# Optimization experiments

Hardware: AMD Instinct MI355X
Metric: run time of the kernel (lower is better)

Reference implementation:

```python
import jax, jax.numpy as jnp
import numpy as np

NUM_HEADS = 16

def setup_inputs() -> dict:
    key = jax.random.key(0)
    ks = jax.random.split(key, 8)
    B, S, X, D = 2, 2048, 1, 1024
    scale = 1.0 / np.sqrt(D)
    return {
        "query": jax.random.normal(ks[0], (B, S, X, D), jnp.float32),
        "key": jax.random.normal(ks[1], (B, S, X, D), jnp.float32),
        "value": jax.random.normal(ks[2], (B, S, X, D), jnp.float32),
        "Wq": jax.random.normal(ks[3], (D, D), jnp.float32) * scale,
        "bq": jnp.zeros((D,), jnp.float32),
        "Wk": jax.random.normal(ks[4], (D, D), jnp.float32) * scale,
        "bk": jnp.zeros((D,), jnp.float32),
        "Wv": jax.random.normal(ks[5], (D, D), jnp.float32) * scale,
        "bv": jnp.zeros((D,), jnp.float32),
        "Wo": jax.random.normal(ks[6], (D, D), jnp.float32) * scale,
        "bo": jnp.zeros((D,), jnp.float32),
    }

def _split_heads(x, B, H):
    # [B, S, X, D] -> [B, H, S*X, depth]
    D = x.shape[-1]
    return x.reshape(B, -1, H, D // H).transpose(0, 2, 1, 3)

def reference(query, key, value, Wq, bq, Wk, bk, Wv, bv, Wo, bo):
    B, S, X, D = query.shape
    H = NUM_HEADS
    q = _split_heads(query @ Wq + bq, B, H)   # [B,H,L,dh], L=S*X
    k = _split_heads(key @ Wk + bk, B, H)
    v = _split_heads(value @ Wv + bv, B, H)
    dh = k.shape[-1]
    logits = jnp.einsum("bhqd,bhkd->bhqk", q, k) / jnp.sqrt(jnp.float32(dh))
    attn = jax.nn.softmax(logits, axis=-1)
    out = jnp.einsum("bhqk,bhkd->bhqd", attn, v)   # [B,H,L,dh]
    out = out.transpose(0, 2, 1, 3).reshape(B, S, -1, D)  # [B,S,X,D]
    return out @ Wo + bo
```

## Files before the change

kernel.cpp:

```cpp
#include <hip/hip_runtime.h>
#include <cstdint>
#include <cstddef>

typedef __bf16 bf16x8 __attribute__((ext_vector_type(8)));
typedef float f32x4 __attribute__((ext_vector_type(4)));
typedef float f32x16 __attribute__((ext_vector_type(16)));
typedef unsigned short u16;
typedef unsigned int u32;

static constexpr int Bn = 2;
static constexpr int L  = 2048;
static constexpr int Dm = 1024;
static constexpr int H  = 16;
static constexpr int DH = 64;
static constexpr int M  = Bn * L;
static constexpr size_t PER = (size_t)Bn * H * L * DH;
static constexpr int NQ = Bn * H * L;

#define SC 0.18033688f

__device__ __forceinline__ u16 f2bf(float f) {
    union { float f; u32 u; } v; v.f = f;
    u32 u = v.u + 0x7FFFu + ((v.u >> 16) & 1u);
    return (u16)(u >> 16);
}

__device__ __forceinline__ u32 pk_bf16(float a, float b) {
#if __has_builtin(__builtin_amdgcn_cvt_pk_bf16_f32)
    typedef __bf16 bf16x2_t __attribute__((ext_vector_type(2)));
    bf16x2_t t = __builtin_amdgcn_cvt_pk_bf16_f32(a, b);
    u32 r; __builtin_memcpy(&r, &t, 4); return r;
#else
    return (u32)f2bf(a) | ((u32)f2bf(b) << 16);
#endif
}
__device__ __forceinline__ u16 f2bf1(float f) { return (u16)(pk_bf16(f, f) & 0xffffu); }

__device__ __forceinline__ void gl2lds16(const void* g, void* l) {
    __builtin_amdgcn_global_load_lds(
        (const __attribute__((address_space(1))) u32*)(uintptr_t)g,
        (__attribute__((address_space(3))) u32*)(uintptr_t)l, 16, 0, 0);
}

__global__ __launch_bounds__(256) void convert_in(
    const float* __restrict__ q, const float* __restrict__ k, const float* __restrict__ v,
    u16* __restrict__ dst)
{
    const float* src = (blockIdx.y == 0) ? q : (blockIdx.y == 1) ? k : v;
    u16* d = dst + (size_t)blockIdx.y * M * Dm;
    const size_t t = (size_t)blockIdx.x * 256 + threadIdx.x;
    const float4* s4 = reinterpret_cast<const float4*>(src) + t * 2;
    float4 f0 = s4[0], f1 = s4[1];
    u32 o[4] = { pk_bf16(f0.x, f0.y), pk_bf16(f0.z, f0.w),
                 pk_bf16(f1.x, f1.y), pk_bf16(f1.z, f1.w) };
    reinterpret_cast<uint4*>(d)[t] = *reinterpret_cast<uint4*>(o);
}

__global__ __launch_bounds__(256) void convert_wt(
    const float* __restrict__ Wq, const float* __restrict__ Wk,
    const float* __restrict__ Wv, const float* __restrict__ Wo,
    u16* __restrict__ dst)
{
    __shared__ u16 Ts[64][72];
    const int z = blockIdx.z;
    const float* W = (z == 0) ? Wq : (z == 1) ? Wk : (z == 2) ? Wv : Wo;
    u16* o = dst + (size_t)z * Dm * Dm;
    const int n0 = blockIdx.x * 64, k0 = blockIdx.y * 64;
    const int tid = threadIdx.x;

    {
        const int kr = tid >> 2, nc = (tid & 3) * 16;
        const float* s = W + (size_t)(k0 + kr) * Dm + n0 + nc;
        const float4* s4 = reinterpret_cast<const float4*>(s);
        float4 a = s4[0], b = s4[1], c = s4[2], d = s4[3];
        u32 t[8] = { pk_bf16(a.x, a.y), pk_bf16(a.z, a.w), pk_bf16(b.x, b.y), pk_bf16(b.z, b.w),
                     pk_bf16(c.x, c.y), pk_bf16(c.z, c.w), pk_bf16(d.x, d.y), pk_bf16(d.z, d.w) };
        *reinterpret_cast<uint4*>(&Ts[kr][nc])     = reinterpret_cast<uint4*>(t)[0];
        *reinterpret_cast<uint4*>(&Ts[kr][nc + 8]) = reinterpret_cast<uint4*>(t)[1];
    }
    __syncthreads();
    {
        const int nr = tid >> 2, kc = (tid & 3) * 16;
        u16 w[16];
        #pragma unroll
        for (int j = 0; j < 16; ++j) w[j] = Ts[kc + j][nr];
        u16* dptr = o + (size_t)(n0 + nr) * Dm + k0 + kc;
        *reinterpret_cast<uint4*>(dptr)     = reinterpret_cast<uint4*>(w)[0];
        *reinterpret_cast<uint4*>(dptr + 8) = reinterpret_cast<uint4*>(w)[1];
    }
}

__global__ __launch_bounds__(256) void gemm_qkv(
    const u16* __restrict__ Abuf, const u16* __restrict__ Wtb,
    const float* __restrict__ bq, const float* __restrict__ bk, const float* __restrict__ bv,
    u16* __restrict__ Qh, u16* __restrict__ Kh, u16* __restrict__ Vth)
{
    __shared__ __align__(16) char smem[36864];

    const int tid = threadIdx.x;
    const int wave = tid >> 6, lane = tid & 63;
    const int quad = lane >> 4, l16 = lane & 15;
    const int wr = wave >> 1, wc = wave & 1;
    const int z = blockIdx.z;
    const u16* A  = Abuf + (size_t)z * M * Dm;
    const u16* Bt = Wtb  + (size_t)z * Dm * Dm;
    const float* bias = (z == 0) ? bq : (z == 1) ? bk : bv;
    u16* out = (z == 0) ? Qh : (z == 1) ? Kh : Vth;
    const int n0 = blockIdx.x * 128, m0 = blockIdx.y * 128;

    const int srow = lane >> 2;
    const int skc  = (lane & 3) * 8;

    f32x4 acc[4][4] = {};

    auto stage = [&](int k0, int bi) {
        #pragma unroll
        for (int i = 0; i < 2; ++i) {
            const int ra = i * 64 + wave * 16;
            gl2lds16(A  + (size_t)(m0 + ra + srow) * Dm + k0 + skc, smem + bi * 8192 + ra * 64);
            gl2lds16(Bt + (size_t)(n0 + ra + srow) * Dm + k0 + skc, smem + 16384 + bi * 8192 + ra * 64);
        }
    };

    stage(0, 0);
    for (int k0 = 0, it = 0; k0 < Dm; k0 += 32, ++it) {
        const int cb = it & 1;
        __syncthreads();
        if (k0 + 32 < Dm) stage(k0 + 32, cb ^ 1);
        const u16* Asb = (const u16*)(smem + cb * 8192);
        const u16* Bsb = (const u16*)(smem + 16384 + cb * 8192);
        bf16x8 af[4], bf[4];
        #pragma unroll
        for (int t = 0; t < 4; ++t) {
            af[t] = *reinterpret_cast<const bf16x8*>(&Asb[(wr * 64 + t * 16 + l16) * 32 + quad * 8]);
            bf[t] = *reinterpret_cast<const bf16x8*>(&Bsb[(wc * 64 + t * 16 + l16) * 32 + quad * 8]);
        }
        #pragma unroll
        for (int mt = 0; mt < 4; ++mt)
            #pragma unroll
            for (int nt = 0; nt < 4; ++nt)
                acc[mt][nt] = __builtin_amdgcn_mfma_f32_16x16x32_bf16(af[mt], bf[nt], acc[mt][nt], 0, 0, 0);
    }

    __syncthreads();
    u16* tile = (u16*)smem + wave * 4608;
    const float qscale = (z == 0) ? SC : 1.0f;
    #pragma unroll
    for (int nt = 0; nt < 4; ++nt) {
        const int n = n0 + wc * 64 + nt * 16 + l16;
        const float badd = bias[n];
        const int cc = nt * 16 + l16;
        #pragma unroll
        for (int mt = 0; mt < 4; ++mt) {
            #pragma unroll
            for (int r = 0; r < 4; ++r) {
                const int rr = mt * 16 + quad * 4 + r;
                const u16 vv = f2bf1((acc[mt][nt][r] + badd) * qscale);
                if (z == 2) tile[cc * 72 + rr] = vv;
                else        tile[rr * 72 + cc] = vv;
            }
        }
    }
    __syncthreads();

    const int rsub = lane >> 3;
    const int csub = (lane & 7) * 8;
    const int h2 = (n0 + wc * 64) >> 6;
    const int mb = m0 + wr * 64;
    const int bb = mb >> 11, ll0 = mb & 2047;
    if (z == 2) {
        const size_t baseV = ((size_t)(bb * H + h2)) * DH * L;
        #pragma unroll
        for (int j = 0; j < 8; ++j) {
            const int d = j * 8 + rsub;
            uint4 vv = *reinterpret_cast<const uint4*>(&tile[d * 72 + csub]);
            *reinterpret_cast<uint4*>(out + baseV + (size_t)d * L + ll0 + csub) = vv;
        }
    } else {
        const size_t base = ((size_t)(bb * H + h2)) * L * DH;
        #pragma unroll
        for (int j = 0; j < 8; ++j) {
            const int row = j * 8 + rsub;
            uint4 vv = *reinterpret_cast<const uint4*>(&tile[row * 72 + csub]);
            *reinterpret_cast<uint4*>(out + base + (size_t)(ll0 + row) * DH + csub) = vv;
        }
    }
}

__global__ __launch_bounds__(256) void attn(
    const u16* __restrict__ Qh, const u16* __restrict__ Kh,
    const u16* __restrict__ Vth, u16* __restrict__ Opart, float* __restrict__ rsums)
{
    __shared__ __align__(16) char smem[32768];
    u16* Os = (u16*)smem;

    const int tid  = threadIdx.x;
    const int wave = tid >> 6, lane = tid & 63;
    const int l31  = lane & 31, hh = lane >> 5;
    const int qt = blockIdx.x >> 1, half = blockIdx.x & 1;
    const int h = blockIdx.y, b = blockIdx.z;
    const size_t hb = ((size_t)(b * H + h)) * L * DH;
    const int q0 = qt * 128 + wave * 32;

    u16*  Op = Opart + (size_t)half * PER;
    float* rp = rsums + (size_t)half * NQ;

    bf16x8 qf[4];
    {
        const u16* qp = Qh + hb + (size_t)(q0 + l31) * DH + hh * 8;
        #pragma unroll
        for (int c = 0; c < 4; ++c)
            qf[c] = *reinterpret_cast<const bf16x8*>(qp + c * 16);
    }

    const int r_off = lane >> 3;
    const int s_sl  = lane & 7;

    auto stage = [&](int kt, int bi) {
        char* base = smem + bi * 16384;
        #pragma unroll
        for (int i = 0; i < 2; ++i) {
            const int rr = wave * 16 + i * 8 + r_off;
            gl2lds16(Kh  + hb + (size_t)(kt * 64 + rr) * DH + ((s_sl ^ (rr & 7)) << 3),
                     base + (wave * 16 + i * 8) * 128);
            gl2lds16(Vth + hb + (size_t)rr * L + kt * 64 + ((s_sl ^ (rr & 7)) << 3),
                     base + 8192 + (wave * 16 + i * 8) * 128);
        }
    };

    int vbK[2], vbV[2];
    #pragma unroll
    for (int t = 0; t < 2; ++t) {
        const int rr = t * 32 + l31;
        vbK[t] = rr * 128 + ((rr & 7) << 4);
        vbV[t] = 8192 + rr * 128 + ((rr & 7) << 4);
    }

    float rsum = 0.f;
    f32x16 oacc[2] = {};

    const int kt0 = half * 16;
    stage(kt0, 0);
    for (int ktl = 0; ktl < 16; ++ktl) {
        const int cb = ktl & 1;
        __syncthreads();
        if (ktl + 1 < 16) stage(kt0 + ktl + 1, cb ^ 1);
        const char* ldsb = smem + cb * 16384;

        f32x16 st[2] = {};
        #pragma unroll
        for (int t = 0; t < 2; ++t) {
            #pragma unroll
            for (int c = 0; c < 4; ++c) {
                bf16x8 kf = *reinterpret_cast<const bf16x8*>(ldsb + (vbK[t] ^ (((c << 1) | hh) << 4)));
                st[t] = __builtin_amdgcn_mfma_f32_32x32x16_bf16(kf, qf[c], st[t], 0, 0, 0);
            }
        }

        bf16x8 pfrag[4];
        #pragma unroll
        for (int t = 0; t < 2; ++t) {
            float p[16];
            #pragma unroll
            for (int rr = 0; rr < 16; ++rr) {
                p[rr] = __builtin_amdgcn_exp2f(st[t][rr]);
                rsum += p[rr];
            }
            #pragma unroll
            for (int g = 0; g < 2; ++g) {
                float* pg = p + g * 8;
                #pragma unroll
                for (int j = 0; j < 4; ++j)
                    asm volatile("v_permlane32_swap_b32 %0, %1" : "+v"(pg[j]), "+v"(pg[j + 4]));
                u32 pkv[4];
                #pragma unroll
                for (int j = 0; j < 4; ++j) pkv[j] = pk_bf16(pg[2 * j], pg[2 * j + 1]);
                pfrag[t * 2 + g] = *reinterpret_cast<bf16x8*>(pkv);
            }
        }

        #pragma unroll
        for (int t = 0; t < 2; ++t) {
            #pragma unroll
            for (int c = 0; c < 4; ++c) {
                bf16x8 vf = *reinterpret_cast<const bf16x8*>(ldsb + (vbV[t] ^ (((c << 1) | hh) << 4)));
                oacc[t] = __builtin_amdgcn_mfma_f32_32x32x16_bf16(vf, pfrag[c], oacc[t], 0, 0, 0);
            }
        }
    }

    rsum += __shfl_xor(rsum, 32);

    #pragma unroll
    for (int pass = 0; pass < 2; ++pass) {
        __syncthreads();
        if ((wave >> 1) == pass) {
            const int qloc = (wave & 1) * 32 + l31;
            #pragma unroll
            for (int t = 0; t < 2; ++t) {
                #pragma unroll
                for (int rq = 0; rq < 4; ++rq) {
                    const int d0 = t * 32 + rq * 8 + hh * 4;
                    *reinterpret_cast<u32*>(&Os[qloc * 72 + d0]) =
                        pk_bf16(oacc[t][rq * 4 + 0], oacc[t][rq * 4 + 1]);
                    *reinterpret_cast<u32*>(&Os[qloc * 72 + d0 + 2]) =
                        pk_bf16(oacc[t][rq * 4 + 2], oacc[t][rq * 4 + 3]);
                }
            }
        }
        __syncthreads();
        {
            const int row = tid >> 2, cc = (tid & 3) * 16;
            u16* dst = Op + hb + (size_t)(qt * 128 + pass * 64 + row) * DH + cc;
            *reinterpret_cast<uint4*>(dst)     = *reinterpret_cast<const uint4*>(&Os[row * 72 + cc]);
            *reinterpret_cast<uint4*>(dst + 8) = *reinterpret_cast<const uint4*>(&Os[row * 72 + cc + 8]);
        }
    }
    if (hh == 0) rp[((size_t)(b * H + h)) * L + q0 + l31] = rsum;
}

__global__ __launch_bounds__(256) void attn_merge(
    const u16* __restrict__ O0, const u16* __restrict__ O1,
    const float* __restrict__ r0, const float* __restrict__ r1,
    u16* __restrict__ ctx)
{
    const int g = blockIdx.x * 256 + threadIdx.x;
    const int row = g >> 3, dc = (g & 7) * 8;
    const int b = row >> 15, h = (row >> 11) & (H - 1), l = row & (L - 1);
    const float inv = 1.0f / (r0[row] + r1[row]);
    bf16x8 a = *reinterpret_cast<const bf16x8*>(O0 + (size_t)row * DH + dc);
    bf16x8 c = *reinterpret_cast<const bf16x8*>(O1 + (size_t)row * DH + dc);
    u32 o[4];
    #pragma unroll
    for (int i = 0; i < 4; ++i)
        o[i] = pk_bf16(((float)a[2 * i] + (float)c[2 * i]) * inv,
                       ((float)a[2 * i + 1] + (float)c[2 * i + 1]) * inv);
    *reinterpret_cast<uint4*>(ctx + ((size_t)(b * L + l)) * Dm + h * DH + dc) =
        *reinterpret_cast<uint4*>(o);
}

__global__ __launch_bounds__(256) void gemm_out(
    const u16* __restrict__ A, const u16* __restrict__ Bt,
    const float* __restrict__ bias, float* __restrict__ out)
{
    __shared__ u16 As[2][128 * 32];
    __shared__ u16 Bs[2][64 * 32];
    const int tid = threadIdx.x;
    const int wave = tid >> 6, lane = tid & 63;
    const int quad = lane >> 4, l16 = lane & 15;
    const int n0 = blockIdx.x * 64, m0 = blockIdx.y * 128;

    const int srow = lane >> 2;
    const int skc  = (lane & 3) * 8;

    f32x4 acc[2][4] = {};

    auto stage = [&](int k0, int bi) {
        #pragma unroll
        for (int i = 0; i < 2; ++i) {
            const int ra = i * 64 + wave * 16;
            gl2lds16(A + (size_t)(m0 + ra + srow) * Dm + k0 + skc, &As[bi][ra * 32]);
        }
        gl2lds16(Bt + (size_t)(n0 + wave * 16 + srow) * Dm + k0 + skc, &Bs[bi][wave * 16 * 32]);
    };

    stage(0, 0);
    for (int k0 = 0, it = 0; k0 < Dm; k0 += 32, ++it) {
        const int cb = it & 1;
        __syncthreads();
        if (k0 + 32 < Dm) stage(k0 + 32, cb ^ 1);
        bf16x8 af[2], bf[4];
        #pragma unroll
        for (int t = 0; t < 2; ++t)
            af[t] = *reinterpret_cast<const bf16x8*>(&As[cb][(wave * 32 + t * 16 + l16) * 32 + quad * 8]);
        #pragma unroll
        for (int t = 0; t < 4; ++t)
            bf[t] = *reinterpret_cast<const bf16x8*>(&Bs[cb][(t * 16 + l16) * 32 + quad * 8]);
        #pragma unroll
        for (int mt = 0; mt < 2; ++mt)
            #pragma unroll
            for (int nt = 0; nt < 4; ++nt)
                acc[mt][nt] = __builtin_amdgcn_mfma_f32_16x16x32_bf16(af[mt], bf[nt], acc[mt][nt], 0, 0, 0);
    }

    #pragma unroll
    for (int nt = 0; nt < 4; ++nt) {
        const int n = n0 + nt * 16 + l16;
        const float badd = bias[n];
        #pragma unroll
        for (int mt = 0; mt < 2; ++mt) {
            #pragma unroll
            for (int r = 0; r < 4; ++r) {
                const int m = m0 + wave * 32 + mt * 16 + quad * 4 + r;
                out[(size_t)m * Dm + n] = acc[mt][nt][r] + badd;
            }
        }
    }
}

extern "C" void kernel_launch(void* const* d_in, const int* in_sizes, int n_in,
                              void* d_out, int out_size, void* d_ws, size_t ws_size,
                              hipStream_t stream) {
    const float* q  = (const float*)d_in[0];
    const float* k  = (const float*)d_in[1];
    const float* v  = (const float*)d_in[2];
    const float* Wq = (const float*)d_in[3];
    const float* bq = (const float*)d_in[4];
    const float* Wk = (const float*)d_in[5];
    const float* bk = (const float*)d_in[6];
    const float* Wv = (const float*)d_in[7];
    const float* bv = (const float*)d_in[8];
    const float* Wo = (const float*)d_in[9];
    const float* bo = (const float*)d_in[10];
    float* out = (float*)d_out;

    u16* Abuf = (u16*)d_ws;
    u16* Wt   = Abuf + 3 * (size_t)M * Dm;
    u16* Qh   = Wt + 4 * (size_t)Dm * Dm;
    u16* Kh   = Qh + PER;
    u16* Vth  = Kh + PER;
    u16* O0   = Vth + PER;
    float* rs = (float*)(O0 + 2 * PER);
    u16* ctx  = Abuf;

    convert_in <<<dim3((M * Dm) / 8 / 256, 3), 256, 0, stream>>>(q, k, v, Abuf);
    convert_wt <<<dim3(Dm / 64, Dm / 64, 4), 256, 0, stream>>>(Wq, Wk, Wv, Wo, Wt);
    gemm_qkv   <<<dim3(Dm / 128, M / 128, 3), 256, 0, stream>>>(Abuf, Wt, bq, bk, bv, Qh, Kh, Vth);
    attn       <<<dim3(L / 128 * 2, H, Bn), 256, 0, stream>>>(Qh, Kh, Vth, O0, rs);
    attn_merge <<<NQ * 8 / 256, 256, 0, stream>>>(O0, O0 + PER, rs, rs + NQ, ctx);
    gemm_out   <<<dim3(Dm / 64, M / 128), 256, 0, stream>>>(ctx, Wt + 3 * (size_t)Dm * Dm, bo, out);
}
```

Baseline: 238.5 us.

## Remap QKV GEMM blocks, compute row sums via MFMA, widen output GEMM tile

The QKV GEMM remaps block indices so that groups of blocks share the same N tile, aiming for better L2 reuse of weights. In attention, the per-row softmax sums are now produced by an extra MFMA against a vector of ones instead of scalar adds. The P repacking converts to bf16 before the permlane swaps, which halves the swaps needed. The output GEMM moves to a 128x128 tile with 512 threads arranged as 4x2 waves, which halves the grid and increases A-tile reuse.

Result: no change. 235.8 us (-1.2%).

```diff
diff --git a/kernel.cpp b/kernel.cpp
--- a/kernel.cpp
+++ b/kernel.cpp
@@ -106,7 +106,11 @@
     const u16* Bt = Wtb  + (size_t)z * Dm * Dm;
     const float* bias = (z == 0) ? bq : (z == 1) ? bk : bv;
     u16* out = (z == 0) ? Qh : (z == 1) ? Kh : Vth;
-    const int n0 = blockIdx.x * 128, m0 = blockIdx.y * 128;
+
+    const int bid = blockIdx.y * 8 + blockIdx.x;
+    const int m_idx = 4 * (bid & 7) + ((bid >> 3) & 3);
+    const int n_idx = bid >> 5;
+    const int n0 = n_idx * 128, m0 = m_idx * 128;
 
     const int srow = lane >> 2;
     const int skc  = (lane & 3) * 8;
@@ -213,6 +217,12 @@
             qf[c] = *reinterpret_cast<const bf16x8*>(qp + c * 16);
     }
 
+    bf16x8 ones;
+    {
+        u32 ov[4] = { 0x3F803F80u, 0x3F803F80u, 0x3F803F80u, 0x3F803F80u };
+        ones = *reinterpret_cast<bf16x8*>(ov);
+    }
+
     const int r_off = lane >> 3;
     const int s_sl  = lane & 7;
 
@@ -236,8 +246,8 @@
         vbV[t] = 8192 + rr * 128 + ((rr & 7) << 4);
     }
 
-    float rsum = 0.f;
     f32x16 oacc[2] = {};
+    f32x16 oaccR = {};
 
     const int kt0 = half * 16;
     stage(kt0, 0);
@@ -262,34 +272,32 @@
         for (int t = 0; t < 2; ++t) {
             float p[16];
             #pragma unroll
-            for (int rr = 0; rr < 16; ++rr) {
+            for (int rr = 0; rr < 16; ++rr)
                 p[rr] = __builtin_amdgcn_exp2f(st[t][rr]);
-                rsum += p[rr];
-            }
             #pragma unroll
             for (int g = 0; g < 2; ++g) {
                 float* pg = p + g * 8;
-                #pragma unroll
-                for (int j = 0; j < 4; ++j)
-                    asm volatile("v_permlane32_swap_b32 %0, %1" : "+v"(pg[j]), "+v"(pg[j + 4]));
-                u32 pkv[4];
-                #pragma unroll
-                for (int j = 0; j < 4; ++j) pkv[j] = pk_bf16(pg[2 * j], pg[2 * j + 1]);
+                u32 w0 = pk_bf16(pg[0], pg[1]);
+                u32 w1 = pk_bf16(pg[2], pg[3]);
+                u32 w2 = pk_bf16(pg[4], pg[5]);
+                u32 w3 = pk_bf16(pg[6], pg[7]);
+                asm volatile("v_permlane32_swap_b32 %0, %1" : "+v"(w0), "+v"(w2));
+                asm volatile("v_permlane32_swap_b32 %0, %1" : "+v"(w1), "+v"(w3));
+                u32 pkv[4] = { w0, w1, w2, w3 };
                 pfrag[t * 2 + g] = *reinterpret_cast<bf16x8*>(pkv);
             }
         }
 
         #pragma unroll
-        for (int t = 0; t < 2; ++t) {
-            #pragma unroll
-            for (int c = 0; c < 4; ++c) {
+        for (int c = 0; c < 4; ++c) {
+            #pragma unroll
+            for (int t = 0; t < 2; ++t) {
                 bf16x8 vf = *reinterpret_cast<const bf16x8*>(ldsb + (vbV[t] ^ (((c << 1) | hh) << 4)));
                 oacc[t] = __builtin_amdgcn_mfma_f32_32x32x16_bf16(vf, pfrag[c], oacc[t], 0, 0, 0);
             }
-        }
-    }
-
-    rsum += __shfl_xor(rsum, 32);
+            oaccR = __builtin_amdgcn_mfma_f32_32x32x16_bf16(ones, pfrag[c], oaccR, 0, 0, 0);
+        }
+    }
 
     #pragma unroll
     for (int pass = 0; pass < 2; ++pass) {
@@ -316,7 +324,7 @@
             *reinterpret_cast<uint4*>(dst + 8) = *reinterpret_cast<const uint4*>(&Os[row * 72 + cc + 8]);
         }
     }
-    if (hh == 0) rp[((size_t)(b * H + h)) * L + q0 + l31] = rsum;
+    if (hh == 0) rp[((size_t)(b * H + h)) * L + q0 + l31] = oaccR[0];
 }
 
 __global__ __launch_bounds__(256) void attn_merge(
@@ -339,16 +347,17 @@
         *reinterpret_cast<uint4*>(o);
 }
 
-__global__ __launch_bounds__(256) void gemm_out(
+__global__ __launch_bounds__(512) void gemm_out(
     const u16* __restrict__ A, const u16* __restrict__ Bt,
     const float* __restrict__ bias, float* __restrict__ out)
 {
     __shared__ u16 As[2][128 * 32];
-    __shared__ u16 Bs[2][64 * 32];
+    __shared__ u16 Bs[2][128 * 32];
     const int tid = threadIdx.x;
     const int wave = tid >> 6, lane = tid & 63;
     const int quad = lane >> 4, l16 = lane & 15;
-    const int n0 = blockIdx.x * 64, m0 = blockIdx.y * 128;
+    const int wr = wave >> 1, wc = wave & 1;
+    const int n0 = blockIdx.x * 128, m0 = blockIdx.y * 128;
 
     const int srow = lane >> 2;
     const int skc  = (lane & 3) * 8;
@@ -356,12 +365,8 @@
     f32x4 acc[2][4] = {};
 
     auto stage = [&](int k0, int bi) {
-        #pragma unroll
-        for (int i = 0; i < 2; ++i) {
-            const int ra = i * 64 + wave * 16;
-            gl2lds16(A + (size_t)(m0 + ra + srow) * Dm + k0 + skc, &As[bi][ra * 32]);
-        }
-        gl2lds16(Bt + (size_t)(n0 + wave * 16 + srow) * Dm + k0 + skc, &Bs[bi][wave * 16 * 32]);
+        gl2lds16(A  + (size_t)(m0 + wave * 16 + srow) * Dm + k0 + skc, &As[bi][(wave * 16) * 32]);
+        gl2lds16(Bt + (size_t)(n0 + wave * 16 + srow) * Dm + k0 + skc, &Bs[bi][(wave * 16) * 32]);
     };
 
     stage(0, 0);
@@ -372,10 +377,10 @@
         bf16x8 af[2], bf[4];
         #pragma unroll
         for (int t = 0; t < 2; ++t)
-            af[t] = *reinterpret_cast<const bf16x8*>(&As[cb][(wave * 32 + t * 16 + l16) * 32 + quad * 8]);
+            af[t] = *reinterpret_cast<const bf16x8*>(&As[cb][(wr * 32 + t * 16 + l16) * 32 + quad * 8]);
         #pragma unroll
         for (int t = 0; t < 4; ++t)
-            bf[t] = *reinterpret_cast<const bf16x8*>(&Bs[cb][(t * 16 + l16) * 32 + quad * 8]);
+            bf[t] = *reinterpret_cast<const bf16x8*>(&Bs[cb][(wc * 64 + t * 16 + l16) * 32 + quad * 8]);
         #pragma unroll
         for (int mt = 0; mt < 2; ++mt)
             #pragma unroll
@@ -385,13 +390,13 @@
 
     #pragma unroll
     for (int nt = 0; nt < 4; ++nt) {
-        const int n = n0 + nt * 16 + l16;
+        const int n = n0 + wc * 64 + nt * 16 + l16;
         const float badd = bias[n];
         #pragma unroll
         for (int mt = 0; mt < 2; ++mt) {
             #pragma unroll
             for (int r = 0; r < 4; ++r) {
-                const int m = m0 + wave * 32 + mt * 16 + quad * 4 + r;
+                const int m = m0 + wr * 32 + mt * 16 + quad * 4 + r;
                 out[(size_t)m * Dm + n] = acc[mt][nt][r] + badd;
             }
         }
@@ -428,5 +433,5 @@
     gemm_qkv   <<<dim3(Dm / 128, M / 128, 3), 256, 0, stream>>>(Abuf, Wt, bq, bk, bv, Qh, Kh, Vth);
     attn       <<<dim3(L / 128 * 2, H, Bn), 256, 0, stream>>>(Qh, Kh, Vth, O0, rs);
     attn_merge <<<NQ * 8 / 256, 256, 0, stream>>>(O0, O0 + PER, rs, rs + NQ, ctx);
-    gemm_out   <<<dim3(Dm / 64, M / 128), 256, 0, stream>>>(ctx, Wt + 3 * (size_t)Dm * Dm, bo, out);
-}
+    gemm_out   <<<dim3(Dm / 128, M / 128), 512, 0, stream>>>(ctx, Wt + 3 * (size_t)Dm * Dm, bo, out);
+}
```
